# Performance work log

Hardware: AMD Instinct MI355X
Metric: run time of the kernel (lower is better)

## Reference

```python
import jax, jax.numpy as jnp
import numpy as np

RES = (32, 32, 32)   # S, H, W
WS = 4               # window size (cubic)
SHIFT = 2            # shift size
NH = 6               # num heads
C = 192              # dim
EPS = 1e-5


def _rel_pos_index(ws):
    coords = np.stack(np.meshgrid(np.arange(ws), np.arange(ws), np.arange(ws), indexing='ij'))
    cf = coords.reshape(3, -1)                      # (3, N)
    rc = (cf[:, :, None] - cf[:, None, :]).transpose(1, 2, 0).astype(np.int64)  # (N,N,3)
    rc[..., 0] += ws - 1
    rc[..., 1] += ws - 1
    rc[..., 2] += ws - 1
    rc[..., 0] *= 3 * ws - 1
    rc[..., 1] *= 2 * ws - 1
    return rc.sum(-1)                               # (N, N)

_RPI = jnp.asarray(_rel_pos_index(WS))


def _ln(x, g, b):
    m = jnp.mean(x, axis=-1, keepdims=True)
    v = jnp.mean(jnp.square(x - m), axis=-1, keepdims=True)
    return (x - m) * jax.lax.rsqrt(v + EPS) * g + b


def setup_inputs():
    key = jax.random.key(0)
    ks = jax.random.split(key, 12)
    B, L = 2, RES[0] * RES[1] * RES[2]
    nW, N = 512, WS ** 3
    Hd = 4 * C
    p = lambda k, s: jax.random.normal(k, s, jnp.float32) * 0.02
    return {
        'x': jax.random.normal(ks[0], (B, L, C), jnp.float32),
        'mask_matrix': jax.random.normal(ks[1], (nW, N, N), jnp.float32),
        'skip': jax.random.normal(ks[2], (B, L, C), jnp.float32),
        'x_up': jax.random.normal(ks[3], (B, L, C), jnp.float32),
        'norm1_g': jnp.ones((C,), jnp.float32), 'norm1_b': jnp.zeros((C,), jnp.float32),
        'kv_w': p(ks[4], (C, 2 * C)), 'kv_b': jnp.zeros((2 * C,), jnp.float32),
        'rpb_table': p(ks[5], ((2 * WS - 1) ** 3, NH)),
        'proj_w': p(ks[6], (C, C)), 'proj_b': jnp.zeros((C,), jnp.float32),
        'norm2_g': jnp.ones((C,), jnp.float32), 'norm2_b': jnp.zeros((C,), jnp.float32),
        'fc1_w': p(ks[7], (C, Hd)), 'fc1_b': jnp.zeros((Hd,), jnp.float32),
        'fc2_w': p(ks[8], (Hd, C)), 'fc2_b': jnp.zeros((C,), jnp.float32),
    }


def reference(x, mask_matrix, skip, x_up, norm1_g, norm1_b, kv_w, kv_b, rpb_table,
              proj_w, proj_b, norm2_g, norm2_b, fc1_w, fc1_b, fc2_w, fc2_b):
    B, L, _ = x.shape
    S, H, W = RES
    ws, N = WS, WS ** 3
    hd = C // NH
    scale = hd ** -0.5

    sn = _ln(skip, norm1_g, norm1_b).reshape(B, S, H, W, C)
    qn = _ln(x_up, norm1_g, norm1_b).reshape(B, S, H, W, C)
    # cyclic shift (shift_size > 0)
    sn = jnp.roll(sn, (-SHIFT, -SHIFT, -SHIFT), axis=(1, 2, 3))
    qn = jnp.roll(qn, (-SHIFT, -SHIFT, -SHIFT), axis=(1, 2, 3))

    def part(t):  # window partition -> (B*nW, N, C)
        t = t.reshape(B, S // ws, ws, H // ws, ws, W // ws, ws, C)
        return t.transpose(0, 1, 3, 5, 2, 4, 6, 7).reshape(-1, N, C)

    skw, qw = part(sn), part(qn)
    B_ = skw.shape[0]

    kv = (skw @ kv_w + kv_b).reshape(B_, N, 2, NH, hd)
    k = kv[:, :, 0].transpose(0, 2, 1, 3)   # (B_, NH, N, hd)
    v = kv[:, :, 1].transpose(0, 2, 1, 3)
    q = qw.reshape(B_, N, NH, hd).transpose(0, 2, 1, 3) * scale

    attn = jnp.einsum('bhqd,bhkd->bhqk', q, k)
    rpb = rpb_table[_RPI.reshape(-1)].reshape(N, N, NH).transpose(2, 0, 1)  # (NH, N, N)
    attn = attn + rpb[None]
    nW = mask_matrix.shape[0]
    attn = attn.reshape(B, nW, NH, N, N) + mask_matrix[None, :, None]
    attn = jax.nn.softmax(attn.reshape(B_, NH, N, N), axis=-1)

    out = jnp.einsum('bhqk,bhkd->bhqd', attn, v).transpose(0, 2, 1, 3).reshape(B_, N, C)
    out = out @ proj_w + proj_b

    # window reverse
    out = out.reshape(B, S // ws, H // ws, W // ws, ws, ws, ws, C)
    out = out.transpose(0, 1, 4, 2, 5, 3, 6, 7).reshape(B, S, H, W, C)
    out = jnp.roll(out, (SHIFT, SHIFT, SHIFT), axis=(1, 2, 3)).reshape(B, L, C)

    x = x + out
    h = _ln(x, norm2_g, norm2_b)
    h = jax.nn.gelu(h @ fc1_w + fc1_b, approximate=False) @ fc2_w + fc2_b
    return x + h
```

## Files before the change

### kernel.cpp

```cpp
#include <hip/hip_runtime.h>
#include <math.h>

typedef unsigned short u16;
typedef __bf16 bf16x8 __attribute__((ext_vector_type(8)));
typedef float f32x4 __attribute__((ext_vector_type(4)));
typedef unsigned short u16x8 __attribute__((ext_vector_type(8)));

#define SHIFT 2

static __device__ __forceinline__ f32x4 mfma16(bf16x8 a, bf16x8 b, f32x4 c) {
  return __builtin_amdgcn_mfma_f32_16x16x32_bf16(a, b, c, 0, 0, 0);
}
static __device__ __forceinline__ u16 f2bf(float f) {
  unsigned u = __builtin_bit_cast(unsigned, f);
  unsigned r = u + 0x7fffu + ((u >> 16) & 1u);
  return (u16)(r >> 16);
}
static __device__ __forceinline__ float bf2f(u16 u) {
  unsigned v = (unsigned)u << 16;
  return __builtin_bit_cast(float, v);
}
static __device__ __forceinline__ void stage16(const u16* g, u16* lbase, int lane) {
#if __has_builtin(__builtin_amdgcn_global_load_lds)
  __builtin_amdgcn_global_load_lds(
      (const __attribute__((address_space(1))) unsigned int*)g,
      (__attribute__((address_space(3))) unsigned int*)lbase, 16, 0, 0);
#else
  *(u16x8*)(lbase + lane * 8) = *(const u16x8*)g;
#endif
}

#define OFF_KVWT  ((size_t)0)
#define OFF_PRWT  (OFF_KVWT + 384*192*2)
#define OFF_FC1WT (OFF_PRWT + 192*192*2)
#define OFF_FC2WT (OFF_FC1WT + 768*192*2)
#define OFF_SKW   (OFF_FC2WT + 192*768*2)
#define OFF_QW    (OFF_SKW + (size_t)65536*192*2)
#define OFF_KVB   (OFF_QW + (size_t)65536*192*2)
#define OFF_POX   (OFF_KVB + (size_t)65536*384*2)
#define OFF_YB    (OFF_POX + (size_t)65536*192*2)
#define OFF_HN    (OFF_YB + (size_t)65536*192*2)
#define OFF_RPBG  (OFF_HN + (size_t)65536*192*2)

__global__ __launch_bounds__(256) void k_prep(
    const float* __restrict__ kv_w, const float* __restrict__ proj_w,
    const float* __restrict__ fc1_w, const float* __restrict__ fc2_w,
    const float* __restrict__ rpb,
    u16* __restrict__ kvT, u16* __restrict__ prT,
    u16* __restrict__ f1T, u16* __restrict__ f2T, u16* __restrict__ rpbg) {
  int i = blockIdx.x * 256 + threadIdx.x;
  if (i < 192 * 384) kvT[(i % 384) * 192 + i / 384] = f2bf(kv_w[i]);
  if (i < 192 * 192) prT[(i % 192) * 192 + i / 192] = f2bf(proj_w[i]);
  if (i < 192 * 768) f1T[(i % 768) * 192 + i / 768] = f2bf(fc1_w[i]);
  if (i < 768 * 192) f2T[(i % 192) * 768 + i / 192] = f2bf(fc2_w[i]);
  if (i < 24576) {
    int h = i >> 12, rem = i & 4095, qr = rem >> 6, kc = rem & 63;
    int qs = qr >> 4, qh = (qr >> 2) & 3, qx = qr & 3;
    int ks = kc >> 4, kh = (kc >> 2) & 3, kx = kc & 3;
    int idx = (qs - ks + 3) * 11 + (qh - kh + 3) * 7 + (qx - kx + 3);
    rpbg[i] = f2bf(rpb[idx * 6 + h]);
  }
}

__global__ __launch_bounds__(256) void k_ln_part(
    const float* __restrict__ skip, const float* __restrict__ x_up,
    const float* __restrict__ gam, const float* __restrict__ bet,
    u16* __restrict__ skw, u16* __restrict__ qw) {
  int row = blockIdx.x * 4 + (threadIdx.x >> 6);
  int lane = threadIdx.x & 63;
  const float* sp = skip + (size_t)row * 192;
  const float* qp = x_up + (size_t)row * 192;
  float sv[3], qv[3], ss = 0.f, qs = 0.f;
#pragma unroll
  for (int j = 0; j < 3; j++) {
    sv[j] = sp[lane + 64 * j]; qv[j] = qp[lane + 64 * j];
    ss += sv[j]; qs += qv[j];
  }
#pragma unroll
  for (int m = 1; m < 64; m <<= 1) { ss += __shfl_xor(ss, m, 64); qs += __shfl_xor(qs, m, 64); }
  float sm = ss * (1.f / 192.f), qm = qs * (1.f / 192.f);
  float s2 = 0.f, q2 = 0.f;
#pragma unroll
  for (int j = 0; j < 3; j++) { float d = sv[j] - sm; s2 += d * d; d = qv[j] - qm; q2 += d * d; }
#pragma unroll
  for (int m = 1; m < 64; m <<= 1) { s2 += __shfl_xor(s2, m, 64); q2 += __shfl_xor(q2, m, 64); }
  float sr = rsqrtf(s2 * (1.f / 192.f) + 1e-5f), qr = rsqrtf(q2 * (1.f / 192.f) + 1e-5f);
  int b = row >> 15, l = row & 32767;
  int s = l >> 10, h = (l >> 5) & 31, w = l & 31;
  int s_ = (s - SHIFT) & 31, h_ = (h - SHIFT) & 31, w_ = (w - SHIFT) & 31;
  int wIdx = ((s_ >> 2) * 8 + (h_ >> 2)) * 8 + (w_ >> 2);
  int n = ((s_ & 3) * 4 + (h_ & 3)) * 4 + (w_ & 3);
  size_t orow = ((size_t)(b * 512 + wIdx) * 64 + n) * 192;
  const float scale = 0.17677669529663687f;
#pragma unroll
  for (int j = 0; j < 3; j++) {
    int cc = lane + 64 * j;
    float gg = gam[cc], bb = bet[cc];
    skw[orow + cc] = f2bf((sv[j] - sm) * sr * gg + bb);
    qw[orow + cc]  = f2bf(((qv[j] - qm) * qr * gg + bb) * scale);
  }
}

__global__ __launch_bounds__(256, 2) void k_kv(
    const u16* __restrict__ A, const u16* __restrict__ BT,
    const float* __restrict__ bias, u16* __restrict__ outh) {
  __shared__ u16 lw[192 * 192];
  int mb = blockIdx.x, nb = blockIdx.y;
  int tid = threadIdx.x, l = tid & 63, wv = tid >> 6, g = l >> 4, c = l & 15;
  int wr = wv >> 1, wc = wv & 1;
#pragma unroll
  for (int i = 0; i < 18; i++) {
    int CI = i * 256 + tid;
    int row = CI / 24, ch = CI % 24;
    int sch = (ch & 24) | ((ch ^ row) & 7);
    stage16(BT + (size_t)(nb * 192 + row) * 192 + sch * 8, lw + (i * 256 + wv * 64) * 8, l);
  }
  __syncthreads();
  f32x4 acc[4][6] = {};
#pragma unroll
  for (int ks = 0; ks < 6; ks++) {
    bf16x8 a[4];
#pragma unroll
    for (int m = 0; m < 4; m++)
      a[m] = *(const bf16x8*)&A[(size_t)(mb * 128 + wr * 64 + m * 16 + c) * 192 + ks * 32 + g * 8];
#pragma unroll
    for (int n = 0; n < 6; n++) {
      int col = wc * 96 + n * 16 + c;
      int ch = ks * 4 + g;
      int chp = (ch & 24) | ((ch ^ col) & 7);
      bf16x8 b = *(const bf16x8*)&lw[col * 192 + chp * 8];
#pragma unroll
      for (int m = 0; m < 4; m++) acc[m][n] = mfma16(a[m], b, acc[m][n]);
    }
  }
#pragma unroll
  for (int n = 0; n < 6; n++)
#pragma unroll
    for (int m = 0; m < 4; m++) {
      int col = nb * 192 + wc * 96 + n * 16 + c;
      float bb = bias[col];
#pragma unroll
      for (int r = 0; r < 4; r++) {
        int row = mb * 128 + wr * 64 + m * 16 + g * 4 + r;
        outh[(size_t)row * 384 + col] = f2bf(acc[m][n][r] + bb);
      }
    }
}

__global__ __launch_bounds__(384) void k_attn_mega(
    const u16* __restrict__ qw, const u16* __restrict__ kvb,
    const u16* __restrict__ rpbg, const float* __restrict__ mask,
    const u16* __restrict__ prT, const float* __restrict__ proj_b,
    u16* __restrict__ pox) {
  __shared__ __align__(16) char smem[38400];
  u16* lv = (u16*)smem;
  u16* lo = (u16*)smem;
  u16* lp = (u16*)(smem + 24576);
  int b_ = blockIdx.x, wIdx = b_ & 511;
  int tid = threadIdx.x, l = tid & 63, wv = tid >> 6, g = l >> 4, c = l & 15;
  int h = wv;
#pragma unroll
  for (int i = 0; i < 4; i++) {
    int CI = i * 384 + tid;
    int row = CI / 24, ch = CI % 24;
    stage16(kvb + ((size_t)b_ * 64 + row) * 384 + 192 + ch * 8,
            lv + (i * 384 + wv * 64) * 8, l);
  }
  const float* mrow = mask + (size_t)wIdx * 4096;
  float4 mv[4][4];
#pragma unroll
  for (int n = 0; n < 4; n++)
#pragma unroll
    for (int m = 0; m < 4; m++)
      mv[n][m] = *(const float4*)&mrow[(n * 16 + c) * 64 + m * 16 + g * 4];
  bf16x8 qa[4], kb[4];
#pragma unroll
  for (int m = 0; m < 4; m++)
    qa[m] = *(const bf16x8*)&qw[((size_t)b_ * 64 + m * 16 + c) * 192 + h * 32 + g * 8];
#pragma unroll
  for (int n = 0; n < 4; n++)
    kb[n] = *(const bf16x8*)&kvb[((size_t)b_ * 64 + n * 16 + c) * 384 + h * 32 + g * 8];
  __syncthreads();
  bf16x8 vb[2][2];
#pragma unroll
  for (int kk = 0; kk < 2; kk++)
#pragma unroll
    for (int nd = 0; nd < 2; nd++) {
      union { u16 u[8]; bf16x8 v; } bb;
#pragma unroll
      for (int j = 0; j < 8; j++)
        bb.u[j] = lv[(kk * 32 + g * 8 + j) * 192 + h * 32 + nd * 16 + c];
      vb[kk][nd] = bb.v;
    }
  __syncthreads();
  f32x4 acc[4][4] = {};
#pragma unroll
  for (int m = 0; m < 4; m++)
#pragma unroll
    for (int n = 0; n < 4; n++) acc[m][n] = mfma16(kb[m], qa[n], acc[m][n]);
  const u16* rg = rpbg + h * 4096;
  f32x4 oacc[4][2] = {};
#pragma unroll
  for (int n = 0; n < 4; n++) {
    ushort4 rv[4];
#pragma unroll
    for (int m = 0; m < 4; m++)
      rv[m] = *(const ushort4*)&rg[(n * 16 + c) * 64 + m * 16 + g * 4];
    float vals[4][4];
    float mx = -3.4e38f;
#pragma unroll
    for (int m = 0; m < 4; m++) {
      float mr[4] = {mv[n][m].x, mv[n][m].y, mv[n][m].z, mv[n][m].w};
      u16 ru[4] = {rv[m].x, rv[m].y, rv[m].z, rv[m].w};
#pragma unroll
      for (int r = 0; r < 4; r++) {
        vals[m][r] = acc[m][n][r] + bf2f(ru[r]) + mr[r];
        mx = fmaxf(mx, vals[m][r]);
      }
    }
    mx = fmaxf(mx, __shfl_xor(mx, 16, 64));
    mx = fmaxf(mx, __shfl_xor(mx, 32, 64));
    float sum = 0.f;
#pragma unroll
    for (int m = 0; m < 4; m++)
#pragma unroll
      for (int r = 0; r < 4; r++) { vals[m][r] = __expf(vals[m][r] - mx); sum += vals[m][r]; }
    sum += __shfl_xor(sum, 16, 64);
    sum += __shfl_xor(sum, 32, 64);
    float inv = 1.f / sum;
#pragma unroll
    for (int m = 0; m < 4; m++) {
      unsigned p0 = f2bf(vals[m][0] * inv) | ((unsigned)f2bf(vals[m][1] * inv) << 16);
      unsigned p1 = f2bf(vals[m][2] * inv) | ((unsigned)f2bf(vals[m][3] * inv) << 16);
      *(uint2*)&lp[h * 1152 + c * 72 + m * 16 + g * 4] = make_uint2(p0, p1);
    }
#pragma unroll
    for (int kk = 0; kk < 2; kk++) {
      bf16x8 pa = *(const bf16x8*)&lp[h * 1152 + c * 72 + kk * 32 + g * 8];
#pragma unroll
      for (int nd = 0; nd < 2; nd++) oacc[n][nd] = mfma16(pa, vb[kk][nd], oacc[n][nd]);
    }
  }
  __syncthreads();
#pragma unroll
  for (int m = 0; m < 4; m++)
#pragma unroll
    for (int nd = 0; nd < 2; nd++)
#pragma unroll
      for (int r = 0; r < 4; r++)
        lo[(m * 16 + g * 4 + r) * 200 + h * 32 + nd * 16 + c] = f2bf(oacc[m][nd][r]);
  __syncthreads();
  f32x4 pacc[4][2] = {};
#pragma unroll
  for (int ks = 0; ks < 6; ks++) {
    bf16x8 pa[4];
#pragma unroll
    for (int m = 0; m < 4; m++)
      pa[m] = *(const bf16x8*)&lo[(m * 16 + c) * 200 + ks * 32 + g * 8];
#pragma unroll
    for (int n = 0; n < 2; n++) {
      bf16x8 pb = *(const bf16x8*)&prT[(size_t)(wv * 32 + n * 16 + c) * 192 + ks * 32 + g * 8];
#pragma unroll
      for (int m = 0; m < 4; m++) pacc[m][n] = mfma16(pa[m], pb, pacc[m][n]);
    }
  }
#pragma unroll
  for (int m = 0; m < 4; m++)
#pragma unroll
    for (int r = 0; r < 4; r++) {
      int tok = m * 16 + g * 4 + r;
#pragma unroll
      for (int n = 0; n < 2; n++) {
        int col = wv * 32 + n * 16 + c;
        pox[((size_t)b_ * 64 + tok) * 192 + col] = f2bf(pacc[m][n][r] + proj_b[col]);
      }
    }
}

__global__ __launch_bounds__(256) void k_ln2(
    const float* __restrict__ x, const u16* __restrict__ pox,
    const float* __restrict__ g2, const float* __restrict__ b2,
    u16* __restrict__ yb, u16* __restrict__ hn) {
  int row = blockIdx.x * 4 + (threadIdx.x >> 6);
  int lane = threadIdx.x & 63;
  int b = row >> 15, ll = row & 32767;
  int s = ll >> 10, hh = (ll >> 5) & 31, w = ll & 31;
  int s_ = (s - SHIFT) & 31, h_ = (hh - SHIFT) & 31, w_ = (w - SHIFT) & 31;
  int wI = ((s_ >> 2) * 8 + (h_ >> 2)) * 8 + (w_ >> 2);
  int n = ((s_ & 3) * 4 + (h_ & 3)) * 4 + (w_ & 3);
  size_t wrow = ((size_t)(b * 512 + wI) * 64 + n) * 192;
  float y[3]; float ss = 0.f, sq = 0.f;
#pragma unroll
  for (int j = 0; j < 3; j++) {
    int cc = lane + 64 * j;
    y[j] = x[(size_t)row * 192 + cc] + bf2f(pox[wrow + cc]);
    ss += y[j]; sq += y[j] * y[j];
  }
#pragma unroll
  for (int m = 1; m < 64; m <<= 1) { ss += __shfl_xor(ss, m, 64); sq += __shfl_xor(sq, m, 64); }
  float mu = ss * (1.f / 192.f);
  float rs = rsqrtf(sq * (1.f / 192.f) - mu * mu + 1e-5f);
#pragma unroll
  for (int j = 0; j < 3; j++) {
    int cc = lane + 64 * j;
    yb[(size_t)row * 192 + cc] = f2bf(y[j]);
    hn[(size_t)row * 192 + cc] = f2bf((y[j] - mu) * rs * g2[cc] + b2[cc]);
  }
}

__global__ __launch_bounds__(512) void k_mlp(
    const u16* __restrict__ hn, const u16* __restrict__ f1T,
    const u16* __restrict__ f2T, const float* __restrict__ b1,
    const float* __restrict__ b2f, const u16* __restrict__ yb,
    float* __restrict__ out) {
  __shared__ u16 lds[33792];
  u16* f1c = lds;
  u16* f2c = lds + 12288;
  u16* h1c = lds + 24576;
  int tid = threadIdx.x, l = tid & 63, wv = tid >> 6, g = l >> 4, c = l & 15;
  size_t tok0 = (size_t)blockIdx.x * 128 + wv * 16;
  u16* tile = h1c + wv * 1152;
  bf16x8 hb[6];
#pragma unroll
  for (int ks = 0; ks < 6; ks++)
    hb[ks] = *(const bf16x8*)&hn[(tok0 + c) * 192 + ks * 32 + g * 8];
#pragma unroll
  for (int i = 0; i < 3; i++) {
    int CI = i * 512 + tid;
    int row = CI / 24, chs = CI % 24;
    int sch = (chs & 24) | ((chs ^ row) & 7);
    stage16(f1T + (size_t)row * 192 + sch * 8, f1c + (i * 512 + wv * 64) * 8, l);
  }
#pragma unroll
  for (int i = 0; i < 3; i++) {
    int CI = i * 512 + tid;
    int row = CI >> 3, chs = CI & 7;
    int sch = chs ^ (row & 7);
    stage16(f2T + (size_t)row * 768 + sch * 8, f2c + (i * 512 + wv * 64) * 8, l);
  }
  __syncthreads();
  f32x4 acc2[12] = {};
#pragma unroll 1
  for (int ko = 0; ko < 12; ko++) {
    f32x4 acc1[4] = {};
#pragma unroll
    for (int ks = 0; ks < 6; ks++) {
      int ch = ks * 4 + g;
      int chp = (ch & 24) | ((ch ^ c) & 7);
#pragma unroll
      for (int cf = 0; cf < 4; cf++) {
        bf16x8 wa = *(const bf16x8*)&f1c[(cf * 16 + c) * 192 + chp * 8];
        acc1[cf] = mfma16(wa, hb[ks], acc1[cf]);
      }
    }
#pragma unroll
    for (int cf = 0; cf < 4; cf++) {
      float4 b1v = *(const float4*)&b1[ko * 64 + cf * 16 + g * 4];
      unsigned pk[2];
#pragma unroll
      for (int p = 0; p < 2; p++) {
        unsigned lohi[2];
#pragma unroll
        for (int q = 0; q < 2; q++) {
          int r = p * 2 + q;
          float v = acc1[cf][r] + (r == 0 ? b1v.x : r == 1 ? b1v.y : r == 2 ? b1v.z : b1v.w);
          float u2 = v * (1.5957691216f + 0.0713548163f * v * v);
          v = v * (1.f / (1.f + __expf(-u2)));
          lohi[q] = f2bf(v);
        }
        pk[p] = lohi[0] | (lohi[1] << 16);
      }
      *(uint2*)&tile[c * 72 + cf * 16 + g * 4] = make_uint2(pk[0], pk[1]);
    }
    __syncthreads();
    if (ko < 11) {
#pragma unroll
      for (int i = 0; i < 3; i++) {
        int CI = i * 512 + tid;
        int row = CI / 24, chs = CI % 24;
        int sch = (chs & 24) | ((chs ^ row) & 7);
        stage16(f1T + (size_t)((ko + 1) * 64 + row) * 192 + sch * 8,
                f1c + (i * 512 + wv * 64) * 8, l);
      }
    }
#pragma unroll
    for (int ck = 0; ck < 2; ck++) {
      bf16x8 a2 = *(const bf16x8*)&tile[c * 72 + ck * 32 + g * 8];
      int ch = ck * 4 + g;
      int chp = ch ^ (c & 7);
#pragma unroll
      for (int of = 0; of < 12; of++) {
        bf16x8 wb = *(const bf16x8*)&f2c[(of * 16 + c) * 64 + chp * 8];
        acc2[of] = mfma16(a2, wb, acc2[of]);
      }
    }
    __syncthreads();
    if (ko < 11) {
#pragma unroll
      for (int i = 0; i < 3; i++) {
        int CI = i * 512 + tid;
        int row = CI >> 3, chs = CI & 7;
        int sch = chs ^ (row & 7);
        stage16(f2T + (size_t)row * 768 + (ko + 1) * 64 + sch * 8,
                f2c + (i * 512 + wv * 64) * 8, l);
      }
    }
  }
#pragma unroll
  for (int of = 0; of < 12; of++) {
    int col = of * 16 + c;
    float bb = b2f[col];
#pragma unroll
    for (int r = 0; r < 4; r++) {
      size_t trow = tok0 + g * 4 + r;
      size_t base = trow * 192 + col;
      out[base] = acc2[of][r] + bb + bf2f(yb[base]);
    }
  }
}

extern "C" void kernel_launch(void* const* d_in, const int* in_sizes, int n_in,
                              void* d_out, int out_size, void* d_ws, size_t ws_size,
                              hipStream_t stream) {
  const float* x      = (const float*)d_in[0];
  const float* mask   = (const float*)d_in[1];
  const float* skip   = (const float*)d_in[2];
  const float* x_up   = (const float*)d_in[3];
  const float* n1g    = (const float*)d_in[4];
  const float* n1b    = (const float*)d_in[5];
  const float* kv_w   = (const float*)d_in[6];
  const float* kv_b   = (const float*)d_in[7];
  const float* rpb    = (const float*)d_in[8];
  const float* proj_w = (const float*)d_in[9];
  const float* proj_b = (const float*)d_in[10];
  const float* n2g    = (const float*)d_in[11];
  const float* n2b    = (const float*)d_in[12];
  const float* fc1_w  = (const float*)d_in[13];
  const float* fc1_b  = (const float*)d_in[14];
  const float* fc2_w  = (const float*)d_in[15];
  const float* fc2_b  = (const float*)d_in[16];
  char* ws = (char*)d_ws;
  u16* kvT  = (u16*)(ws + OFF_KVWT);
  u16* prT  = (u16*)(ws + OFF_PRWT);
  u16* f1T  = (u16*)(ws + OFF_FC1WT);
  u16* f2T  = (u16*)(ws + OFF_FC2WT);
  u16* skw  = (u16*)(ws + OFF_SKW);
  u16* qw   = (u16*)(ws + OFF_QW);
  u16* kvb  = (u16*)(ws + OFF_KVB);
  u16* pox  = (u16*)(ws + OFF_POX);
  u16* yb   = (u16*)(ws + OFF_YB);
  u16* hn   = (u16*)(ws + OFF_HN);
  u16* rpbg = (u16*)(ws + OFF_RPBG);
  float* out = (float*)d_out;

  k_prep<<<dim3(576), dim3(256), 0, stream>>>(kv_w, proj_w, fc1_w, fc2_w, rpb,
                                              kvT, prT, f1T, f2T, rpbg);
  k_ln_part<<<dim3(16384), dim3(256), 0, stream>>>(skip, x_up, n1g, n1b, skw, qw);
  k_kv<<<dim3(512, 2), dim3(256), 0, stream>>>(skw, kvT, kv_b, kvb);
  k_attn_mega<<<dim3(1024), dim3(384), 0, stream>>>(
      qw, kvb, rpbg, mask, prT, proj_b, pox);
  k_ln2<<<dim3(16384), dim3(256), 0, stream>>>(x, pox, n2g, n2b, yb, hn);
  k_mlp<<<dim3(512), dim3(512), 0, stream>>>(
      hn, f1T, f2T, fc1_b, fc2_b, yb, out);
}
```

Measured before the change: 229.8 us.

## Double-buffer fc1 weights in LDS and read fc2 weights directly from global

The MLP kernel now ping-pongs the fc1 weight chunk between two LDS buffers. The next chunk is prefetched before the GELU epilogue, which removes one of the two block barriers per iteration. The fc2 weights are no longer staged in LDS and are loaded straight from global memory (through cache) inside the MFMA loop. The GELU sigmoid form is rewritten with exp2f and pre-scaled constants. The change trades LDS staging and a barrier for uncoalesced-ish global loads of fc2 weights on every iteration.

```diff
diff --git a/kernel.cpp b/kernel.cpp
--- a/kernel.cpp
+++ b/kernel.cpp
@@ -314,8 +314,6 @@
     const float* __restrict__ b2f, const u16* __restrict__ yb,
     float* __restrict__ out) {
   __shared__ u16 lds[33792];
-  u16* f1c = lds;
-  u16* f2c = lds + 12288;
   u16* h1c = lds + 24576;
   int tid = threadIdx.x, l = tid & 63, wv = tid >> 6, g = l >> 4, c = l & 15;
   size_t tok0 = (size_t)blockIdx.x * 128 + wv * 16;
@@ -329,19 +327,13 @@
     int CI = i * 512 + tid;
     int row = CI / 24, chs = CI % 24;
     int sch = (chs & 24) | ((chs ^ row) & 7);
-    stage16(f1T + (size_t)row * 192 + sch * 8, f1c + (i * 512 + wv * 64) * 8, l);
-  }
-#pragma unroll
-  for (int i = 0; i < 3; i++) {
-    int CI = i * 512 + tid;
-    int row = CI >> 3, chs = CI & 7;
-    int sch = chs ^ (row & 7);
-    stage16(f2T + (size_t)row * 768 + sch * 8, f2c + (i * 512 + wv * 64) * 8, l);
+    stage16(f1T + (size_t)row * 192 + sch * 8, lds + (i * 512 + wv * 64) * 8, l);
   }
   __syncthreads();
   f32x4 acc2[12] = {};
 #pragma unroll 1
   for (int ko = 0; ko < 12; ko++) {
+    const u16* f1c = lds + (ko & 1) * 12288;
     f32x4 acc1[4] = {};
 #pragma unroll
     for (int ks = 0; ks < 6; ks++) {
@@ -353,58 +345,46 @@
         acc1[cf] = mfma16(wa, hb[ks], acc1[cf]);
       }
     }
-#pragma unroll
-    for (int cf = 0; cf < 4; cf++) {
-      float4 b1v = *(const float4*)&b1[ko * 64 + cf * 16 + g * 4];
-      unsigned pk[2];
-#pragma unroll
-      for (int p = 0; p < 2; p++) {
-        unsigned lohi[2];
-#pragma unroll
-        for (int q = 0; q < 2; q++) {
-          int r = p * 2 + q;
-          float v = acc1[cf][r] + (r == 0 ? b1v.x : r == 1 ? b1v.y : r == 2 ? b1v.z : b1v.w);
-          float u2 = v * (1.5957691216f + 0.0713548163f * v * v);
-          v = v * (1.f / (1.f + __expf(-u2)));
-          lohi[q] = f2bf(v);
-        }
-        pk[p] = lohi[0] | (lohi[1] << 16);
-      }
-      *(uint2*)&tile[c * 72 + cf * 16 + g * 4] = make_uint2(pk[0], pk[1]);
-    }
-    __syncthreads();
     if (ko < 11) {
+      u16* nbuf = lds + ((ko + 1) & 1) * 12288;
 #pragma unroll
       for (int i = 0; i < 3; i++) {
         int CI = i * 512 + tid;
         int row = CI / 24, chs = CI % 24;
         int sch = (chs & 24) | ((chs ^ row) & 7);
         stage16(f1T + (size_t)((ko + 1) * 64 + row) * 192 + sch * 8,
-                f1c + (i * 512 + wv * 64) * 8, l);
-      }
+                nbuf + (i * 512 + wv * 64) * 8, l);
+      }
+    }
+#pragma unroll
+    for (int cf = 0; cf < 4; cf++) {
+      float4 b1v = *(const float4*)&b1[ko * 64 + cf * 16 + g * 4];
+      unsigned pk[2];
+#pragma unroll
+      for (int p = 0; p < 2; p++) {
+        unsigned lohi[2];
+#pragma unroll
+        for (int q = 0; q < 2; q++) {
+          int r = p * 2 + q;
+          float v = acc1[cf][r] + (r == 0 ? b1v.x : r == 1 ? b1v.y : r == 2 ? b1v.z : b1v.w);
+          float u2 = v * (2.3022652f + 0.10295394f * v * v);
+          v = v * (1.f / (1.f + exp2f(-u2)));
+          lohi[q] = f2bf(v);
+        }
+        pk[p] = lohi[0] | (lohi[1] << 16);
+      }
+      *(uint2*)&tile[c * 72 + cf * 16 + g * 4] = make_uint2(pk[0], pk[1]);
     }
 #pragma unroll
     for (int ck = 0; ck < 2; ck++) {
       bf16x8 a2 = *(const bf16x8*)&tile[c * 72 + ck * 32 + g * 8];
-      int ch = ck * 4 + g;
-      int chp = ch ^ (c & 7);
 #pragma unroll
       for (int of = 0; of < 12; of++) {
-        bf16x8 wb = *(const bf16x8*)&f2c[(of * 16 + c) * 64 + chp * 8];
+        bf16x8 wb = *(const bf16x8*)&f2T[(size_t)(of * 16 + c) * 768 + ko * 64 + ck * 32 + g * 8];
         acc2[of] = mfma16(a2, wb, acc2[of]);
       }
     }
     __syncthreads();
-    if (ko < 11) {
-#pragma unroll
-      for (int i = 0; i < 3; i++) {
-        int CI = i * 512 + tid;
-        int row = CI >> 3, chs = CI & 7;
-        int sch = chs ^ (row & 7);
-        stage16(f2T + (size_t)row * 768 + (ko + 1) * 64 + sch * 8,
-                f2c + (i * 512 + wv * 64) * 8, l);
-      }
-    }
   }
 #pragma unroll
   for (int of = 0; of < 12; of++) {
```

Result: slower. 331.9 us (+44.4%).
